# Kernel tuning notes

Measured on AMD Instinct MI355X. Metric: run time of the kernel, lower is better.

The kernel has to match this reference:

```python
import jax, jax.numpy as jnp
import numpy as np

B, S, D, H, AD, E = 4, 2048, 1024, 2048, 128, 8

def _ln(x, g, b, eps=1e-5):
    m = jnp.mean(x, axis=-1, keepdims=True)
    v = jnp.var(x, axis=-1, keepdims=True)
    return (x - m) * jax.lax.rsqrt(v + eps) * g + b

def setup_inputs() -> dict:
    key = jax.random.key(0)
    ks = jax.random.split(key, 12)
    scale = 1.0 / D ** 0.5
    ascale = scale * 0.01
    ead = 0.01 / AD ** 0.5
    return {
        'x': jax.random.normal(ks[0], (B, S, D), jnp.float32),
        'expert_weights': jax.random.uniform(ks[1], (B, S, E), jnp.float32),
        'Wu': jax.random.normal(ks[2], (H, D), jnp.float32) * scale,
        'bu': jnp.zeros((H,), jnp.float32),
        'Wg': jax.random.normal(ks[3], (H, D), jnp.float32) * scale,
        'bg': jnp.zeros((H,), jnp.float32),
        'Wd': jax.random.normal(ks[4], (D, H), jnp.float32) * scale,
        'bd': jnp.zeros((D,), jnp.float32),
        'Wpre': jax.random.normal(ks[5], (AD, D), jnp.float32) * ascale,
        'bpre': jnp.zeros((AD,), jnp.float32),
        'Wpost': jax.random.normal(ks[6], (AD, H), jnp.float32) * ascale,
        'bpost': jnp.zeros((AD,), jnp.float32),
        'ln_g': jnp.ones((AD,), jnp.float32),
        'ln_b': jnp.zeros((AD,), jnp.float32),
        'Wap': jax.random.normal(ks[7], (H, AD), jnp.float32) * ascale,
        'A': jax.random.normal(ks[8], (E, AD, AD), jnp.float32) * ead,
        'eg': jnp.ones((E, AD), jnp.float32),
        'eb': jnp.zeros((E, AD), jnp.float32),
        'Wp': jax.random.normal(ks[9], (H, AD), jnp.float32) * ead,
        'Wo': jax.random.normal(ks[10], (D, H), jnp.float32) * ead,
    }

def reference(x, expert_weights, Wu, bu, Wg, bg, Wd, bd, Wpre, bpre, Wpost, bpost, ln_g, ln_b, Wap, A, eg, eb, Wp, Wo):
    # ---- SharedExpertMLP ----
    up = x @ Wu.T + bu                      # [B,S,H]
    gate = x @ Wg.T + bg
    hidden = jax.nn.silu(gate) * up
    adapt_in = _ln(x @ Wpre.T + bpre, ln_g, ln_b)        # [B,S,AD]
    adapt_out = _ln(hidden @ Wpost.T + bpost, ln_g, ln_b)
    aw = jnp.einsum('bsa,bta->bst', adapt_in, adapt_out)  # [B,S,S]
    aw = jax.nn.silu(jnp.clip(aw, -5.0, 5.0))
    adapt = jnp.einsum('bst,bta->bsa', aw, adapt_in)
    hidden = hidden + 0.1 * (adapt @ Wap.T)
    shared = hidden @ Wd.T + bd                           # [B,S,D]
    # ---- expert branch (vectorized over experts) ----
    pre = x @ Wpre.T + bpre                               # [B,S,AD] (no adapt_norm here, as in torch)
    h = jnp.einsum('bsa,eca->ebsc', pre, A)               # per-expert adapter linear
    h = _ln(h, eg[:, None, None, :], eb[:, None, None, :])
    wmask = jnp.where(expert_weights > 0, expert_weights, 0.0)  # [B,S,E]
    hw = jnp.einsum('ebsa,bse->bsa', h, wmask)            # weighted combine before shared projections
    Wc = Wo @ Wp                                          # [D,AD]: output_proj(expert_proj(.))
    contrib = hw @ Wc.T                                   # [B,S,D]
    # sum_i w_i * (shared + 0.1*mask_i*expert_i) = shared*sum(w) + 0.1*sum(w_i*expert_i)
    return shared * jnp.sum(expert_weights, axis=-1, keepdims=True) + 0.1 * contrib
```

## Files before the change

### kernel.cpp

```cpp
#include <hip/hip_runtime.h>
#include <math.h>

#define BB 4
#define SS 2048
#define DD 1024
#define HH 2048
#define AD 128
#define EE 8
#define MM (BB*SS)
#define PS 136

typedef unsigned short u16;
typedef short bf16x8 __attribute__((ext_vector_type(8)));
typedef float f32x4 __attribute__((ext_vector_type(4)));
typedef float f32x16 __attribute__((ext_vector_type(16)));

__device__ __forceinline__ float silu_f(float x){ return x / (1.f + __expf(-x)); }

__device__ __forceinline__ u16 f2bf(float f){
    union { float f; unsigned u; } c; c.f = f;
    unsigned r = (c.u + 0x7FFFu + ((c.u >> 16) & 1u)) >> 16;
    return (u16)r;
}

__device__ __forceinline__ void gld16(const u16* g, u16* l){
    __builtin_amdgcn_global_load_lds((const __attribute__((address_space(1))) void*)g,
                                     (__attribute__((address_space(3))) void*)l, 16, 0, 0);
}

#define VMCNT(n) asm volatile("s_waitcnt vmcnt(" #n ")" ::: "memory")

__global__ __launch_bounds__(256,2) void mfma_sk(
    const u16* __restrict__ A, const u16* __restrict__ B, float* __restrict__ P,
    int M, int K, int S, long sA, long sB, long sC, long sSplit)
{
    __shared__ __align__(16) u16 As[128*32];
    __shared__ __align__(16) u16 Bs[128*32];
    const int t = threadIdx.x;
    const int lane = t & 63;
    const int wv = t >> 6;
    const int s = blockIdx.x;
    const int m0 = blockIdx.y * 128;
    const u16* Ab = A + (long)blockIdx.z * sA;
    const u16* Bb = B + (long)blockIdx.z * sB;
    const int srow = t >> 2, scol = (t & 3) * 8;
    const int Ks = K / S, kBeg = s * Ks;
    const u16* ga0 = Ab + (long)(m0 + srow) * K + scol + kBeg;
    const u16* ga1 = ga0 + 64L * K;
    const u16* gb0 = Bb + (long)srow * K + scol + kBeg;
    const u16* gb1 = gb0 + 64L * K;
    u16* la0 = As + t * 8;  u16* la1 = As + 2048 + t * 8;
    u16* lb0 = Bs + t * 8;  u16* lb1 = Bs + 2048 + t * 8;
    const int fr = lane & 15, q = lane >> 4;
    const int wm = (wv & 1) * 64, wn = (wv >> 1) * 64;

    f32x4 acc[4][4] = {};
    for (int k0 = 0; k0 < Ks; k0 += 32) {
        gld16(ga0 + k0, la0);
        gld16(ga1 + k0, la1);
        gld16(gb0 + k0, lb0);
        gld16(gb1 + k0, lb1);
        __syncthreads();
        bf16x8 af[4], bfr[4];
        #pragma unroll
        for (int i = 0; i < 4; ++i) af[i]  = *(const bf16x8*)&As[(wm + i*16 + fr)*32 + q*8];
        #pragma unroll
        for (int i = 0; i < 4; ++i) bfr[i] = *(const bf16x8*)&Bs[(wn + i*16 + fr)*32 + q*8];
        #pragma unroll
        for (int mi = 0; mi < 4; ++mi)
            #pragma unroll
            for (int ni = 0; ni < 4; ++ni)
                acc[mi][ni] = __builtin_amdgcn_mfma_f32_16x16x32_bf16(af[mi], bfr[ni], acc[mi][ni], 0, 0, 0);
        __syncthreads();
    }

    float* Pf = P + (long)s * sSplit + (long)blockIdx.z * sC;
    #pragma unroll
    for (int mi = 0; mi < 4; ++mi)
        #pragma unroll
        for (int ni = 0; ni < 4; ++ni) {
            const int col = wn + ni*16 + fr;
            #pragma unroll
            for (int r = 0; r < 4; ++r) {
                const int row = m0 + wm + mi*16 + q*4 + r;
                Pf[(long)row * 128 + col] = acc[mi][ni][r];
            }
        }
}

__global__ __launch_bounds__(512,2) void mfma_upgate(
    const u16* __restrict__ X, const u16* __restrict__ Wu_, const u16* __restrict__ Wg_,
    const float* __restrict__ bu, const float* __restrict__ bg, u16* __restrict__ H)
{
    __shared__ __align__(16) u16 lds[65536];
    const int t = threadIdx.x, lane = t & 63, wv = t >> 6;
    const int l31 = lane & 31, kh = lane >> 5;
    const int wr = wv >> 2, wc = wv & 3;
    const int m0 = blockIdx.y * 256, n0 = blockIdx.x * 128;

    const int srow = t >> 2;
    const int gcol = (((t & 3) ^ ((t >> 3) & 3)) * 8);
    const u16* gx0 = X   + (long)(m0 + srow) * DD + gcol;
    const u16* gx1 = gx0 + 128L * DD;
    const u16* gu  = Wu_ + (long)(n0 + srow) * DD + gcol;
    const u16* gg  = Wg_ + (long)(n0 + srow) * DD + gcol;
    const int st8 = t * 8;

    const int sw3 = (l31 >> 1) & 3;
    int offA[4][2], offB[2];
    #pragma unroll
    for (int m = 0; m < 4; ++m)
        #pragma unroll
        for (int ks = 0; ks < 2; ++ks)
            offA[m][ks] = (wr*128 + m*32 + l31)*32 + (((ks*2 + kh) ^ sw3) * 8);
    #pragma unroll
    for (int ks = 0; ks < 2; ++ks)
        offB[ks] = (wc*32 + l31)*32 + (((ks*2 + kh) ^ sw3) * 8);

    f32x16 accU[4] = {};
    f32x16 accG[4] = {};

    auto stage = [&](int tb) {
        u16* Lb = lds + (tb & 3) * 16384;
        const int k0 = tb * 32;
        gld16(gx0 + k0, Lb + st8);
        gld16(gx1 + k0, Lb + 4096 + st8);
        gld16(gu  + k0, Lb + 8192 + st8);
        gld16(gg  + k0, Lb + 12288 + st8);
    };

    auto compute = [&](int tb) {
        const u16* Lb = lds + (tb & 3) * 16384;
        bf16x8 a[4][2], uf[2], gf[2];
        #pragma unroll
        for (int ks = 0; ks < 2; ++ks) {
            uf[ks] = *(const bf16x8*)&Lb[8192  + offB[ks]];
            gf[ks] = *(const bf16x8*)&Lb[12288 + offB[ks]];
        }
        #pragma unroll
        for (int m = 0; m < 4; ++m)
            #pragma unroll
            for (int ks = 0; ks < 2; ++ks)
                a[m][ks] = *(const bf16x8*)&Lb[offA[m][ks]];
        __builtin_amdgcn_s_setprio(1);
        #pragma unroll
        for (int m = 0; m < 4; ++m)
            #pragma unroll
            for (int ks = 0; ks < 2; ++ks) {
                accU[m] = __builtin_amdgcn_mfma_f32_32x32x16_bf16(a[m][ks], uf[ks], accU[m], 0, 0, 0);
                accG[m] = __builtin_amdgcn_mfma_f32_32x32x16_bf16(a[m][ks], gf[ks], accG[m], 0, 0, 0);
            }
        __builtin_amdgcn_s_setprio(0);
    };

    stage(0); stage(1); stage(2);

    #pragma unroll 1
    for (int tt = 0; tt < 29; ++tt) {
        VMCNT(8);
        __builtin_amdgcn_s_barrier();
        __builtin_amdgcn_sched_barrier(0);
        stage(tt + 3);
        compute(tt);
    }
    VMCNT(8);
    __builtin_amdgcn_s_barrier();
    __builtin_amdgcn_sched_barrier(0);
    compute(29);
    VMCNT(4);
    __builtin_amdgcn_s_barrier();
    __builtin_amdgcn_sched_barrier(0);
    compute(30);
    VMCNT(0);
    __builtin_amdgcn_s_barrier();
    __builtin_amdgcn_sched_barrier(0);
    compute(31);

    const int col = n0 + wc*32 + l31;
    const float bub = bu[col], bgb = bg[col];
    u16* Hp = H + (long)(m0 + wr*128) * HH + col;
    #pragma unroll
    for (int m = 0; m < 4; ++m)
        #pragma unroll
        for (int r = 0; r < 16; ++r) {
            const int rowl = m*32 + (r & 3) + 8*(r >> 2) + 4*kh;
            const float u = accU[m][r] + bub;
            const float g = accG[m][r] + bgb;
            Hp[(long)rowl * HH] = f2bf(silu_f(g) * u);
        }
}

__global__ __launch_bounds__(512,2) void mfma_final(
    const u16* __restrict__ Hh, const u16* __restrict__ Wd_,
    const u16* __restrict__ Ac, const u16* __restrict__ Wcat,
    const float* __restrict__ bd, const float* __restrict__ sumw,
    float* __restrict__ out)
{
    __shared__ __align__(16) u16 lds[49152];
    const int t = threadIdx.x, lane = t & 63, wv = t >> 6;
    const int l31 = lane & 31, kh = lane >> 5;
    const int wr = wv >> 2, wc = wv & 3;
    const int m0 = blockIdx.y * 256, n0 = blockIdx.x * 128;

    const int r0 = t >> 2;
    const int gcol = (((t & 3) ^ ((t >> 3) & 3)) * 8);
    const u16* gA1 = Hh   + (long)(m0 + r0) * HH  + gcol;
    const u16* gB1 = Wd_  + (long)(n0 + r0) * HH  + gcol;
    const u16* gA2 = Ac   + (long)(m0 + r0) * 256 + gcol;
    const u16* gB2 = Wcat + (long)(n0 + r0) * 256 + gcol;
    const int st8 = t * 8;

    const int sw3 = (l31 >> 1) & 3;
    int offA[4][2], offB[2];
    #pragma unroll
    for (int m = 0; m < 4; ++m)
        #pragma unroll
        for (int ks = 0; ks < 2; ++ks)
            offA[m][ks] = (wr*128 + m*32 + l31)*32 + (((ks*2 + kh) ^ sw3) * 8);
    #pragma unroll
    for (int ks = 0; ks < 2; ++ks)
        offB[ks] = 8192 + (wc*32 + l31)*32 + (((ks*2 + kh) ^ sw3) * 8);

    f32x16 acc[4]  = {};
    f32x16 acc2[4] = {};

    auto stage = [&](int tk) {
        u16* Lb = lds + (tk & 3) * 12288;
        if (tk < 64) {
            const int k0 = tk * 32;
            gld16(gA1 + k0,             Lb + st8);
            gld16(gA1 + 128L*HH + k0,   Lb + 4096 + st8);
            gld16(gB1 + k0,             Lb + 8192 + st8);
        } else {
            const int k0 = (tk - 64) * 32;
            gld16(gA2 + k0,             Lb + st8);
            gld16(gA2 + 128L*256 + k0,  Lb + 4096 + st8);
            gld16(gB2 + k0,             Lb + 8192 + st8);
        }
    };

    auto compute = [&](int tk, f32x16 (&A)[4]) {
        const u16* Lb = lds + (tk & 3) * 12288;
        bf16x8 a[4][2], b[2];
        #pragma unroll
        for (int ks = 0; ks < 2; ++ks) b[ks] = *(const bf16x8*)&Lb[offB[ks]];
        #pragma unroll
        for (int m = 0; m < 4; ++m)
            #pragma unroll
            for (int ks = 0; ks < 2; ++ks)
                a[m][ks] = *(const bf16x8*)&Lb[offA[m][ks]];
        __builtin_amdgcn_s_setprio(1);
        #pragma unroll
        for (int m = 0; m < 4; ++m)
            #pragma unroll
            for (int ks = 0; ks < 2; ++ks)
                A[m] = __builtin_amdgcn_mfma_f32_32x32x16_bf16(a[m][ks], b[ks], A[m], 0, 0, 0);
        __builtin_amdgcn_s_setprio(0);
    };

    stage(0); stage(1); stage(2);
    #pragma unroll 1
    for (int tt = 0; tt < 69; ++tt) {
        VMCNT(6);
        __builtin_amdgcn_s_barrier();
        __builtin_amdgcn_sched_barrier(0);
        stage(tt + 3);
        if (tt < 64) compute(tt, acc); else compute(tt, acc2);
    }
    VMCNT(6);
    __builtin_amdgcn_s_barrier();
    __builtin_amdgcn_sched_barrier(0);
    compute(69, acc2);
    VMCNT(3);
    __builtin_amdgcn_s_barrier();
    __builtin_amdgcn_sched_barrier(0);
    compute(70, acc2);
    VMCNT(0);
    __builtin_amdgcn_s_barrier();
    __builtin_amdgcn_sched_barrier(0);
    compute(71, acc2);

    const int col = n0 + wc*32 + l31;
    const float bdc = bd[col];
    #pragma unroll
    for (int m = 0; m < 4; ++m)
        #pragma unroll
        for (int r = 0; r < 16; ++r) {
            const int row = m0 + wr*128 + m*32 + (r & 3) + 8*(r >> 2) + 4*kh;
            out[(long)row * DD + col] =
                sumw[row] * (acc[m][r] + bdc) + 0.1f * acc2[m][r];
        }
}

__global__ __launch_bounds__(256,2) void flash_pv(
    const u16* __restrict__ ai, const u16* __restrict__ ao,
    const u16* __restrict__ aiT, float* __restrict__ adaptP)
{
    __shared__ __align__(16) u16 As[128*32];
    __shared__ __align__(16) u16 Bs[128*32];
    __shared__ __align__(16) u16 Psh[128*PS];
    const int t = threadIdx.x, lane = t & 63, wv = t >> 6;
    const int fr = lane & 15, q = lane >> 4;
    const int wm = (wv & 1) * 64, wn = (wv >> 1) * 64;
    const int tg = blockIdx.x, s0 = blockIdx.y * 128, b = blockIdx.z;
    const u16* aib  = ai  + (long)b * SS * AD;
    const u16* aob  = ao  + (long)b * SS * AD;
    const u16* aiTb = aiT + (long)b * AD * SS;
    const int srow = t >> 2, scol = (t & 3) * 8;
    u16* la0 = As + t * 8;  u16* la1 = As + 2048 + t * 8;
    u16* lb0 = Bs + t * 8;  u16* lb1 = Bs + 2048 + t * 8;
    const u16* ga0 = aib + (long)(s0 + srow) * AD + scol;
    const u16* ga1 = ga0 + 64L * AD;

    f32x4 vacc[4][4] = {};
    for (int ti = 0; ti < 2; ++ti) {
        const int t0 = tg * 256 + ti * 128;
        const u16* gb0 = aob + (long)(t0 + srow) * AD + scol;
        const u16* gb1 = gb0 + 64L * AD;
        f32x4 acc[4][4] = {};
        for (int k0 = 0; k0 < AD; k0 += 32) {
            gld16(ga0 + k0, la0);
            gld16(ga1 + k0, la1);
            gld16(gb0 + k0, lb0);
            gld16(gb1 + k0, lb1);
            __syncthreads();
            bf16x8 af[4], bfr[4];
            #pragma unroll
            for (int i = 0; i < 4; ++i) af[i]  = *(const bf16x8*)&As[(wm + i*16 + fr)*32 + q*8];
            #pragma unroll
            for (int i = 0; i < 4; ++i) bfr[i] = *(const bf16x8*)&Bs[(wn + i*16 + fr)*32 + q*8];
            #pragma unroll
            for (int mi = 0; mi < 4; ++mi)
                #pragma unroll
                for (int ni = 0; ni < 4; ++ni)
                    acc[mi][ni] = __builtin_amdgcn_mfma_f32_16x16x32_bf16(af[mi], bfr[ni], acc[mi][ni], 0, 0, 0);
            __syncthreads();
        }
        #pragma unroll
        for (int mi = 0; mi < 4; ++mi)
            #pragma unroll
            for (int ni = 0; ni < 4; ++ni)
                #pragma unroll
                for (int r = 0; r < 4; ++r) {
                    float v = acc[mi][ni][r];
                    v = fminf(fmaxf(v, -5.f), 5.f);
                    Psh[(wm + mi*16 + q*4 + r)*PS + wn + ni*16 + fr] = f2bf(silu_f(v));
                }
        __syncthreads();
        #pragma unroll
        for (int kk = 0; kk < 4; ++kk) {
            bf16x8 pf[4], bi[4];
            #pragma unroll
            for (int mi = 0; mi < 4; ++mi)
                pf[mi] = *(const bf16x8*)&Psh[(wm + mi*16 + fr)*PS + kk*32 + q*8];
            #pragma unroll
            for (int ni = 0; ni < 4; ++ni)
                bi[ni] = *(const bf16x8*)&aiTb[(long)(wn + ni*16 + fr)*SS + t0 + kk*32 + q*8];
            #pragma unroll
            for (int mi = 0; mi < 4; ++mi)
                #pragma unroll
                for (int ni = 0; ni < 4; ++ni)
                    vacc[mi][ni] = __builtin_amdgcn_mfma_f32_16x16x32_bf16(pf[mi], bi[ni], vacc[mi][ni], 0, 0, 0);
        }
    }
    float* Pf = adaptP + (long)tg * MM * AD + (long)(b * SS + s0) * AD;
    #pragma unroll
    for (int mi = 0; mi < 4; ++mi)
        #pragma unroll
        for (int ni = 0; ni < 4; ++ni) {
            const int col = wn + ni*16 + fr;
            #pragma unroll
            for (int r = 0; r < 4; ++r) {
                const int row = wm + mi*16 + q*4 + r;
                Pf[(long)row * AD + col] = vacc[mi][ni][r];
            }
        }
}

__global__ __launch_bounds__(256) void scale_adapt(
    const float* __restrict__ P, const float* __restrict__ sumw, u16* __restrict__ acat)
{
    const int i = blockIdx.x * 256 + threadIdx.x;
    float4 v = ((const float4*)P)[i];
    #pragma unroll
    for (int tg = 1; tg < 8; ++tg) {
        const float4 w = ((const float4*)P)[i + (long)tg * (MM*AD/4)];
        v.x += w.x; v.y += w.y; v.z += w.z; v.w += w.w;
    }
    const long grow = i >> 5;
    const float sw = sumw[grow];
    ushort4 o;
    o.x = f2bf(sw*v.x); o.y = f2bf(sw*v.y); o.z = f2bf(sw*v.z); o.w = f2bf(sw*v.w);
    ((ushort4*)acat)[grow*64 + 32 + (i & 31)] = o;
}

__global__ __launch_bounds__(256) void expert_fused(
    const u16* __restrict__ pre, const u16* __restrict__ aexp,
    const float* __restrict__ ew, const float* __restrict__ eg,
    const float* __restrict__ eb, u16* __restrict__ acat,
    float* __restrict__ sumw)
{
    __shared__ float ewsh[64*8];
    __shared__ float egsh[8*128], ebsh[8*128];
    const int t = threadIdx.x, lane = t & 63, wv = t >> 6;
    const int fr = lane & 15, q = lane >> 4;
    const int wm = wv * 16;
    const int m0 = blockIdx.x * 64;
    if (t < 128) {
        const int row = t >> 1, j = (t & 1)*4;
        *(float4*)&ewsh[row*8+j] = *(const float4*)&ew[(long)(m0+row)*EE + j];
    }
    {   const int e = t >> 5, c = (t & 31)*4;
        *(float4*)&egsh[e*128+c] = *(const float4*)&eg[e*128+c];
        *(float4*)&ebsh[e*128+c] = *(const float4*)&eb[e*128+c]; }
    __syncthreads();

    f32x4 hwacc[8] = {};
    for (int e = 0; e < EE; ++e) {
        f32x4 acc[8] = {};
        const u16* Ae = aexp + (long)e * AD * AD;
        #pragma unroll
        for (int ks = 0; ks < 4; ++ks) {
            bf16x8 af, bfr[8];
            af = *(const bf16x8*)&pre[(long)(m0 + wm + fr)*AD + ks*32 + q*8];
            #pragma unroll
            for (int ni = 0; ni < 8; ++ni)
                bfr[ni] = *(const bf16x8*)&Ae[(long)(ni*16 + fr)*AD + ks*32 + q*8];
            #pragma unroll
            for (int ni = 0; ni < 8; ++ni)
                acc[ni] = __builtin_amdgcn_mfma_f32_16x16x32_bf16(af, bfr[ni], acc[ni], 0, 0, 0);
        }
        #pragma unroll
        for (int r = 0; r < 4; ++r) {
            float s = 0.f, s2 = 0.f;
            #pragma unroll
            for (int ni = 0; ni < 8; ++ni) { const float v = acc[ni][r]; s += v; s2 += v*v; }
            #pragma unroll
            for (int msk = 1; msk < 16; msk <<= 1) {
                s  += __shfl_xor(s,  msk, 64);
                s2 += __shfl_xor(s2, msk, 64);
            }
            const float mean = s * (1.f/128.f);
            const float var  = s2 * (1.f/128.f) - mean*mean;
            const float rs   = rsqrtf(var + 1e-5f);
            const int rowl = wm + q*4 + r;
            float w = ewsh[rowl*8 + e]; w = w > 0.f ? w : 0.f;
            #pragma unroll
            for (int ni = 0; ni < 8; ++ni) {
                const int col = ni*16 + fr;
                hwacc[ni][r] += w * ((acc[ni][r] - mean) * rs * egsh[e*128+col] + ebsh[e*128+col]);
            }
        }
    }
    #pragma unroll
    for (int r = 0; r < 4; ++r) {
        const int rowl = wm + q*4 + r;
        #pragma unroll
        for (int ni = 0; ni < 8; ++ni)
            acat[(long)(m0+rowl)*256 + ni*16 + fr] = f2bf(hwacc[ni][r]);
        if (fr == 0) {
            float sw = 0.f;
            #pragma unroll
            for (int j = 0; j < 8; ++j) sw += ewsh[rowl*8 + j];
            sumw[m0 + rowl] = sw;
        }
    }
}

template<int S>
__global__ __launch_bounds__(128) void ln_reduce(
    const float* __restrict__ P, long sSplit, const float* __restrict__ bias,
    u16* __restrict__ raw, u16* __restrict__ ln_out,
    const float* __restrict__ g, const float* __restrict__ b)
{
    const int r = blockIdx.x, tid = threadIdx.x;
    float v = bias[tid];
    #pragma unroll
    for (int s = 0; s < S; ++s) v += P[(long)s * sSplit + (long)r * AD + tid];
    if (raw) raw[(long)r * AD + tid] = f2bf(v);
    __shared__ float red[AD], red2[AD];
    red[tid] = v; red2[tid] = v*v;
    __syncthreads();
    for (int s = 64; s > 0; s >>= 1) {
        if (tid < s) { red[tid] += red[tid+s]; red2[tid] += red2[tid+s]; }
        __syncthreads();
    }
    const float mean = red[0] * (1.f/AD);
    const float var  = red2[0] * (1.f/AD) - mean*mean;
    const float rs   = rsqrtf(var + 1e-5f);
    ln_out[(long)r * AD + tid] = f2bf((v - mean) * rs * g[tid] + b[tid]);
}

__global__ __launch_bounds__(256) void reduce_cat(
    const float* __restrict__ P, u16* __restrict__ Wcat)
{
    const int i = blockIdx.x * 256 + threadIdx.x;
    const int a4 = i & 31, z = (i >> 5) & 1, d = i >> 6;
    const float* src = P + (long)z * (4L*DD*AD) + (long)d * AD + a4*4;
    float4 v = *(const float4*)src;
    #pragma unroll
    for (int s = 1; s < 4; ++s) {
        const float4 w = *(const float4*)(src + (long)s * DD * AD);
        v.x += w.x; v.y += w.y; v.z += w.z; v.w += w.w;
    }
    ushort4 o; o.x=f2bf(v.x); o.y=f2bf(v.y); o.z=f2bf(v.z); o.w=f2bf(v.w);
    ((ushort4*)Wcat)[(long)d*64 + z*32 + a4] = o;
}

__global__ __launch_bounds__(256) void transpose6(
    const u16* __restrict__ wRaw, u16* __restrict__ wT,
    const u16* __restrict__ ai, u16* __restrict__ aiT)
{
    __shared__ u16 tile[32][33];
    const int z = blockIdx.z;
    const u16* in; u16* out;
    if (z < 2) { in = wRaw + (long)z * HH * AD; out = wT + (long)z * AD * HH; }
    else       { in = ai + (long)(z-2) * SS * AD; out = aiT + (long)(z-2) * AD * SS; }
    const int x0 = blockIdx.x * 32, y0 = blockIdx.y * 32;
    const int tx = threadIdx.x & 31, ty = threadIdx.x >> 5;
    #pragma unroll
    for (int j = 0; j < 4; ++j)
        tile[ty + j*8][tx] = in[(long)(y0 + ty + j*8) * AD + x0 + tx];
    __syncthreads();
    #pragma unroll
    for (int j = 0; j < 4; ++j)
        out[(long)(x0 + ty + j*8) * SS + y0 + tx] = tile[tx][ty + j*8];
}

struct Cvt5 { const float* in[5]; u16* out[5]; long cum[6]; };
__global__ __launch_bounds__(256) void cvt_pack(Cvt5 a)
{
    const long i = (long)blockIdx.x * 256 + threadIdx.x;
    if (i >= a.cum[5]) return;
    int s = 0;
    while (i >= a.cum[s+1]) ++s;
    const long j = i - a.cum[s];
    const float4 v = ((const float4*)a.in[s])[j];
    ushort4 o;
    o.x = f2bf(v.x); o.y = f2bf(v.y); o.z = f2bf(v.z); o.w = f2bf(v.w);
    ((ushort4*)a.out[s])[j] = o;
}

extern "C" void kernel_launch(void* const* d_in, const int* in_sizes, int n_in,
                              void* d_out, int out_size, void* d_ws, size_t ws_size,
                              hipStream_t stream) {
    const float* x    = (const float*)d_in[0];
    const float* ew   = (const float*)d_in[1];
    const float* Wu   = (const float*)d_in[2];
    const float* bu   = (const float*)d_in[3];
    const float* Wg   = (const float*)d_in[4];
    const float* bg   = (const float*)d_in[5];
    const float* Wd   = (const float*)d_in[6];
    const float* bd   = (const float*)d_in[7];
    const float* Wpre = (const float*)d_in[8];
    const float* bpre = (const float*)d_in[9];
    const float* Wpost= (const float*)d_in[10];
    const float* bpost= (const float*)d_in[11];
    const float* ln_g = (const float*)d_in[12];
    const float* ln_b = (const float*)d_in[13];
    const float* Wap  = (const float*)d_in[14];
    const float* Aex  = (const float*)d_in[15];
    const float* eg   = (const float*)d_in[16];
    const float* eb   = (const float*)d_in[17];
    const float* Wp   = (const float*)d_in[18];
    const float* Wo   = (const float*)d_in[19];
    float* out = (float*)d_out;

    char* p = (char*)d_ws;
    auto take = [&](long bytes) -> char* {
        char* r = p; p += (bytes + 255) & ~255L; return r;
    };
    u16* x_slot  = (u16*)take(16777216);
    u16* wslot   = (u16*)take((long)2*DD*HH*2);
    u16* wpre    = (u16*)take((long)AD*DD*2);
    u16* aex     = (u16*)take((long)EE*AD*AD*2);
    u16* pre_bf  = (u16*)take((long)MM*AD*2);
    u16* ai_bf   = (u16*)take((long)MM*AD*2);
    char* shareA = take(33554432);
    u16* acat    = (u16*)take((long)MM*256*2);
    float* sumw  = (float*)take((long)MM*4);
    u16* hidden  = (u16*)take((long)MM*HH*2);

    u16* x_bf    = x_slot;
    u16* aiT     = x_slot;
    u16* wRaw    = aiT  + 1048576;
    u16* wT      = wRaw + 524288;
    u16* wpost_w = wT   + 524288;
    u16* wcat    = wpost_w + 262144;
    u16* ao_bf   = wcat + 262144;
    float* wcP   = (float*)(ao_bf + 1048576);
    float* preP   = (float*)shareA;
    float* wpostP = (float*)shareA;
    float* adaptP = (float*)shareA;

    {
        Cvt5 a;
        a.in[0]=x;    a.out[0]=x_bf;              long n0=(long)MM*DD/4;
        a.in[1]=Wu;   a.out[1]=wslot;             long n1=(long)HH*DD/4;
        a.in[2]=Wg;   a.out[2]=wslot+(long)DD*HH; long n2=(long)HH*DD/4;
        a.in[3]=Wpre; a.out[3]=wpre;              long n3=(long)AD*DD/4;
        a.in[4]=Aex;  a.out[4]=aex;               long n4=(long)EE*AD*AD/4;
        a.cum[0]=0; a.cum[1]=n0; a.cum[2]=n0+n1; a.cum[3]=n0+n1+n2;
        a.cum[4]=n0+n1+n2+n3; a.cum[5]=n0+n1+n2+n3+n4;
        cvt_pack<<<dim3((a.cum[5]+255)/256), 256, 0, stream>>>(a);
    }
    mfma_sk<<<dim3(4, MM/128, 1), 256, 0, stream>>>(
        x_bf, wpre, preP, MM, DD, 4, 0, 0, 0, (long)MM*AD);
    ln_reduce<4><<<dim3(MM), 128, 0, stream>>>(preP, (long)MM*AD, bpre, pre_bf, ai_bf, ln_g, ln_b);
    expert_fused<<<dim3(MM/64), 256, 0, stream>>>(pre_bf, aex, ew, eg, eb, acat, sumw);
    mfma_upgate<<<dim3(HH/128, MM/256), 512, 0, stream>>>(
        x_bf, wslot, wslot+(long)DD*HH, bu, bg, hidden);
    {
        Cvt5 a;
        a.in[0]=Wo;    a.out[0]=wslot;             long n0=(long)DD*HH/4;
        a.in[1]=Wd;    a.out[1]=wslot+(long)DD*HH; long n1=(long)DD*HH/4;
        a.in[2]=Wpost; a.out[2]=wpost_w;           long n2=(long)AD*HH/4;
        a.in[3]=Wp;    a.out[3]=wRaw;              long n3=(long)HH*AD/4;
        a.in[4]=Wap;   a.out[4]=wRaw+(long)HH*AD;  long n4=(long)HH*AD/4;
        a.cum[0]=0; a.cum[1]=n0; a.cum[2]=n0+n1; a.cum[3]=n0+n1+n2;
        a.cum[4]=n0+n1+n2+n3; a.cum[5]=n0+n1+n2+n3+n4;
        cvt_pack<<<dim3((a.cum[5]+255)/256), 256, 0, stream>>>(a);
    }
    transpose6<<<dim3(4,64,6), 256, 0, stream>>>(wRaw, wT, ai_bf, aiT);
    mfma_sk<<<dim3(4, DD/128, 2), 256, 0, stream>>>(
        wslot, wT, wcP, DD, HH, 4, (long)DD*HH, (long)AD*HH, 4L*DD*AD, (long)DD*AD);
    reduce_cat<<<dim3(256), 256, 0, stream>>>(wcP, wcat);
    mfma_sk<<<dim3(8, MM/128, 1), 256, 0, stream>>>(
        hidden, wpost_w, wpostP, MM, HH, 8, 0, 0, 0, (long)MM*AD);
    ln_reduce<8><<<dim3(MM), 128, 0, stream>>>(wpostP, (long)MM*AD, bpost, nullptr, ao_bf, ln_g, ln_b);
    flash_pv<<<dim3(8, SS/128, BB), 256, 0, stream>>>(ai_bf, ao_bf, aiT, adaptP);
    scale_adapt<<<dim3((long)MM*AD/4/256), 256, 0, stream>>>(adaptP, sumw, acat);
    mfma_final<<<dim3(DD/128, MM/256), 512, 0, stream>>>(
        hidden, wslot+(long)DD*HH, acat, wcat, bd, sumw, out);
}
```

Baseline: 424.2 us.

## Shrink GEMM tiles, split expert loop across waves, raise split-K for Wc

The up/gate and final GEMMs move from 256x128 tiles with 512 threads and a 4-stage LDS pipeline to 128x128 tiles with 256 threads and a 3-stage pipeline. Each wave now computes a 2x2 grid of 32x32 MFMA outputs, so the grid has more blocks and each block uses less LDS. The expert kernel halves rows per block and splits the 8 experts across two wave groups, combining their partial sums through shared memory. The Wc = Wo@Wp split-K GEMM goes from 4 to 16 splits, with reduce_cat summing 16 partials. The trade is more parallelism and occupancy against less operand reuse per tile, more global traffic and extra partial-sum work.

Result: faster. 398.4 us (-6.1%).

```diff
diff --git a/kernel.cpp b/kernel.cpp
--- a/kernel.cpp
+++ b/kernel.cpp
@@ -88,86 +88,87 @@
         }
 }
 
-__global__ __launch_bounds__(512,2) void mfma_upgate(
+__global__ __launch_bounds__(256,2) void mfma_upgate(
     const u16* __restrict__ X, const u16* __restrict__ Wu_, const u16* __restrict__ Wg_,
     const float* __restrict__ bu, const float* __restrict__ bg, u16* __restrict__ H)
 {
-    __shared__ __align__(16) u16 lds[65536];
+    __shared__ __align__(16) u16 lds[36864];
     const int t = threadIdx.x, lane = t & 63, wv = t >> 6;
     const int l31 = lane & 31, kh = lane >> 5;
-    const int wr = wv >> 2, wc = wv & 3;
-    const int m0 = blockIdx.y * 256, n0 = blockIdx.x * 128;
+    const int wr = wv & 1, wc = wv >> 1;
+    const int m0 = blockIdx.y * 128, n0 = blockIdx.x * 128;
 
     const int srow = t >> 2;
     const int gcol = (((t & 3) ^ ((t >> 3) & 3)) * 8);
-    const u16* gx0 = X   + (long)(m0 + srow) * DD + gcol;
-    const u16* gx1 = gx0 + 128L * DD;
-    const u16* gu  = Wu_ + (long)(n0 + srow) * DD + gcol;
-    const u16* gg  = Wg_ + (long)(n0 + srow) * DD + gcol;
+    const u16* gx = X   + (long)(m0 + srow) * DD + gcol;
+    const u16* gu = Wu_ + (long)(n0 + srow) * DD + gcol;
+    const u16* gg = Wg_ + (long)(n0 + srow) * DD + gcol;
     const int st8 = t * 8;
 
     const int sw3 = (l31 >> 1) & 3;
-    int offA[4][2], offB[2];
-    #pragma unroll
-    for (int m = 0; m < 4; ++m)
-        #pragma unroll
-        for (int ks = 0; ks < 2; ++ks)
-            offA[m][ks] = (wr*128 + m*32 + l31)*32 + (((ks*2 + kh) ^ sw3) * 8);
-    #pragma unroll
-    for (int ks = 0; ks < 2; ++ks)
-        offB[ks] = (wc*32 + l31)*32 + (((ks*2 + kh) ^ sw3) * 8);
-
-    f32x16 accU[4] = {};
-    f32x16 accG[4] = {};
+    int offA[2][2], offU[2][2], offG[2][2];
+    #pragma unroll
+    for (int m = 0; m < 2; ++m)
+        #pragma unroll
+        for (int ks = 0; ks < 2; ++ks) {
+            const int ko = ((ks*2 + kh) ^ sw3) * 8;
+            offA[m][ks] =        (wr*64 + m*32 + l31)*32 + ko;
+            offU[m][ks] = 4096 + (wc*64 + m*32 + l31)*32 + ko;
+            offG[m][ks] = 8192 + (wc*64 + m*32 + l31)*32 + ko;
+        }
+
+    f32x16 accU[2][2] = {};
+    f32x16 accG[2][2] = {};
 
     auto stage = [&](int tb) {
-        u16* Lb = lds + (tb & 3) * 16384;
+        u16* Lb = lds + (tb % 3) * 12288;
         const int k0 = tb * 32;
-        gld16(gx0 + k0, Lb + st8);
-        gld16(gx1 + k0, Lb + 4096 + st8);
-        gld16(gu  + k0, Lb + 8192 + st8);
-        gld16(gg  + k0, Lb + 12288 + st8);
+        gld16(gx + k0,           Lb + st8);
+        gld16(gx + 64L*DD + k0,  Lb + 2048 + st8);
+        gld16(gu + k0,           Lb + 4096 + st8);
+        gld16(gu + 64L*DD + k0,  Lb + 6144 + st8);
+        gld16(gg + k0,           Lb + 8192 + st8);
+        gld16(gg + 64L*DD + k0,  Lb + 10240 + st8);
     };
 
     auto compute = [&](int tb) {
-        const u16* Lb = lds + (tb & 3) * 16384;
-        bf16x8 a[4][2], uf[2], gf[2];
-        #pragma unroll
-        for (int ks = 0; ks < 2; ++ks) {
-            uf[ks] = *(const bf16x8*)&Lb[8192  + offB[ks]];
-            gf[ks] = *(const bf16x8*)&Lb[12288 + offB[ks]];
-        }
-        #pragma unroll
-        for (int m = 0; m < 4; ++m)
+        const u16* Lb = lds + (tb % 3) * 12288;
+        bf16x8 a[2][2], uf[2][2], gf[2][2];
+        #pragma unroll
+        for (int n = 0; n < 2; ++n)
+            #pragma unroll
+            for (int ks = 0; ks < 2; ++ks) {
+                uf[n][ks] = *(const bf16x8*)&Lb[offU[n][ks]];
+                gf[n][ks] = *(const bf16x8*)&Lb[offG[n][ks]];
+            }
+        #pragma unroll
+        for (int m = 0; m < 2; ++m)
             #pragma unroll
             for (int ks = 0; ks < 2; ++ks)
                 a[m][ks] = *(const bf16x8*)&Lb[offA[m][ks]];
         __builtin_amdgcn_s_setprio(1);
         #pragma unroll
-        for (int m = 0; m < 4; ++m)
-            #pragma unroll
-            for (int ks = 0; ks < 2; ++ks) {
-                accU[m] = __builtin_amdgcn_mfma_f32_32x32x16_bf16(a[m][ks], uf[ks], accU[m], 0, 0, 0);
-                accG[m] = __builtin_amdgcn_mfma_f32_32x32x16_bf16(a[m][ks], gf[ks], accG[m], 0, 0, 0);
-            }
+        for (int m = 0; m < 2; ++m)
+            #pragma unroll
+            for (int n = 0; n < 2; ++n)
+                #pragma unroll
+                for (int ks = 0; ks < 2; ++ks) {
+                    accU[m][n] = __builtin_amdgcn_mfma_f32_32x32x16_bf16(a[m][ks], uf[n][ks], accU[m][n], 0, 0, 0);
+                    accG[m][n] = __builtin_amdgcn_mfma_f32_32x32x16_bf16(a[m][ks], gf[n][ks], accG[m][n], 0, 0, 0);
+                }
         __builtin_amdgcn_s_setprio(0);
     };
 
-    stage(0); stage(1); stage(2);
-
+    stage(0); stage(1);
     #pragma unroll 1
-    for (int tt = 0; tt < 29; ++tt) {
-        VMCNT(8);
+    for (int tt = 0; tt < 30; ++tt) {
+        VMCNT(6);
         __builtin_amdgcn_s_barrier();
         __builtin_amdgcn_sched_barrier(0);
-        stage(tt + 3);
+        stage(tt + 2);
         compute(tt);
     }
-    VMCNT(8);
-    __builtin_amdgcn_s_barrier();
-    __builtin_amdgcn_sched_barrier(0);
-    compute(29);
-    VMCNT(4);
+    VMCNT(6);
     __builtin_amdgcn_s_barrier();
     __builtin_amdgcn_sched_barrier(0);
     compute(30);
@@ -176,102 +177,104 @@
     __builtin_amdgcn_sched_barrier(0);
     compute(31);
 
-    const int col = n0 + wc*32 + l31;
-    const float bub = bu[col], bgb = bg[col];
-    u16* Hp = H + (long)(m0 + wr*128) * HH + col;
-    #pragma unroll
-    for (int m = 0; m < 4; ++m)
-        #pragma unroll
-        for (int r = 0; r < 16; ++r) {
-            const int rowl = m*32 + (r & 3) + 8*(r >> 2) + 4*kh;
-            const float u = accU[m][r] + bub;
-            const float g = accG[m][r] + bgb;
-            Hp[(long)rowl * HH] = f2bf(silu_f(g) * u);
-        }
-}
-
-__global__ __launch_bounds__(512,2) void mfma_final(
+    #pragma unroll
+    for (int n = 0; n < 2; ++n) {
+        const int col = n0 + wc*64 + n*32 + l31;
+        const float bub = bu[col], bgb = bg[col];
+        #pragma unroll
+        for (int m = 0; m < 2; ++m)
+            #pragma unroll
+            for (int r = 0; r < 16; ++r) {
+                const int row = m0 + wr*64 + m*32 + (r & 3) + 8*(r >> 2) + 4*kh;
+                const float u = accU[m][n][r] + bub;
+                const float g = accG[m][n][r] + bgb;
+                H[(long)row * HH + col] = f2bf(silu_f(g) * u);
+            }
+    }
+}
+
+__global__ __launch_bounds__(256,2) void mfma_final(
     const u16* __restrict__ Hh, const u16* __restrict__ Wd_,
     const u16* __restrict__ Ac, const u16* __restrict__ Wcat,
     const float* __restrict__ bd, const float* __restrict__ sumw,
     float* __restrict__ out)
 {
-    __shared__ __align__(16) u16 lds[49152];
+    __shared__ __align__(16) u16 lds[24576];
     const int t = threadIdx.x, lane = t & 63, wv = t >> 6;
     const int l31 = lane & 31, kh = lane >> 5;
-    const int wr = wv >> 2, wc = wv & 3;
-    const int m0 = blockIdx.y * 256, n0 = blockIdx.x * 128;
-
-    const int r0 = t >> 2;
+    const int wr = wv & 1, wc = wv >> 1;
+    const int m0 = blockIdx.y * 128, n0 = blockIdx.x * 128;
+
+    const int srow = t >> 2;
     const int gcol = (((t & 3) ^ ((t >> 3) & 3)) * 8);
-    const u16* gA1 = Hh   + (long)(m0 + r0) * HH  + gcol;
-    const u16* gB1 = Wd_  + (long)(n0 + r0) * HH  + gcol;
-    const u16* gA2 = Ac   + (long)(m0 + r0) * 256 + gcol;
-    const u16* gB2 = Wcat + (long)(n0 + r0) * 256 + gcol;
+    const u16* gA1 = Hh   + (long)(m0 + srow) * HH  + gcol;
+    const u16* gB1 = Wd_  + (long)(n0 + srow) * HH  + gcol;
+    const u16* gA2 = Ac   + (long)(m0 + srow) * 256 + gcol;
+    const u16* gB2 = Wcat + (long)(n0 + srow) * 256 + gcol;
     const int st8 = t * 8;
 
     const int sw3 = (l31 >> 1) & 3;
-    int offA[4][2], offB[2];
-    #pragma unroll
-    for (int m = 0; m < 4; ++m)
-        #pragma unroll
-        for (int ks = 0; ks < 2; ++ks)
-            offA[m][ks] = (wr*128 + m*32 + l31)*32 + (((ks*2 + kh) ^ sw3) * 8);
-    #pragma unroll
-    for (int ks = 0; ks < 2; ++ks)
-        offB[ks] = 8192 + (wc*32 + l31)*32 + (((ks*2 + kh) ^ sw3) * 8);
-
-    f32x16 acc[4]  = {};
-    f32x16 acc2[4] = {};
+    int offA[2][2], offB[2][2];
+    #pragma unroll
+    for (int m = 0; m < 2; ++m)
+        #pragma unroll
+        for (int ks = 0; ks < 2; ++ks) {
+            const int ko = ((ks*2 + kh) ^ sw3) * 8;
+            offA[m][ks] =        (wr*64 + m*32 + l31)*32 + ko;
+            offB[m][ks] = 4096 + (wc*64 + m*32 + l31)*32 + ko;
+        }
+
+    f32x16 acc[2][2]  = {};
+    f32x16 acc2[2][2] = {};
 
     auto stage = [&](int tk) {
-        u16* Lb = lds + (tk & 3) * 12288;
+        u16* Lb = lds + (tk % 3) * 8192;
         if (tk < 64) {
             const int k0 = tk * 32;
-            gld16(gA1 + k0,             Lb + st8);
-            gld16(gA1 + 128L*HH + k0,   Lb + 4096 + st8);
-            gld16(gB1 + k0,             Lb + 8192 + st8);
+            gld16(gA1 + k0,           Lb + st8);
+            gld16(gA1 + 64L*HH + k0,  Lb + 2048 + st8);
+            gld16(gB1 + k0,           Lb + 4096 + st8);
+            gld16(gB1 + 64L*HH + k0,  Lb + 6144 + st8);
         } else {
             const int k0 = (tk - 64) * 32;
-            gld16(gA2 + k0,             Lb + st8);
-            gld16(gA2 + 128L*256 + k0,  Lb + 4096 + st8);
-            gld16(gB2 + k0,             Lb + 8192 + st8);
+            gld16(gA2 + k0,           Lb + st8);
+            gld16(gA2 + 64L*256 + k0, Lb + 2048 + st8);
+            gld16(gB2 + k0,           Lb + 4096 + st8);
+            gld16(gB2 + 64L*256 + k0, Lb + 6144 + st8);
         }
     };
 
-    auto compute = [&](int tk, f32x16 (&A)[4]) {
-        const u16* Lb = lds + (tk & 3) * 12288;
-        bf16x8 a[4][2], b[2];
-        #pragma unroll
-        for (int ks = 0; ks < 2; ++ks) b[ks] = *(const bf16x8*)&Lb[offB[ks]];
-        #pragma unroll
-        for (int m = 0; m < 4; ++m)
-            #pragma unroll
-            for (int ks = 0; ks < 2; ++ks)
+    auto compute = [&](int tk, f32x16 (&A)[2][2]) {
+        const u16* Lb = lds + (tk % 3) * 8192;
+        bf16x8 a[2][2], b[2][2];
+        #pragma unroll
+        for (int m = 0; m < 2; ++m)
+            #pragma unroll
+            for (int ks = 0; ks < 2; ++ks) {
                 a[m][ks] = *(const bf16x8*)&Lb[offA[m][ks]];
+                b[m][ks] = *(const bf16x8*)&Lb[offB[m][ks]];
+            }
         __builtin_amdgcn_s_setprio(1);
         #pragma unroll
-        for (int m = 0; m < 4; ++m)
-            #pragma unroll
-            for (int ks = 0; ks < 2; ++ks)
-                A[m] = __builtin_amdgcn_mfma_f32_32x32x16_bf16(a[m][ks], b[ks], A[m], 0, 0, 0);
+        for (int m = 0; m < 2; ++m)
+            #pragma unroll
+            for (int n = 0; n < 2; ++n)
+                #pragma unroll
+                for (int ks = 0; ks < 2; ++ks)
+                    A[m][n] = __builtin_amdgcn_mfma_f32_32x32x16_bf16(a[m][ks], b[n][ks], A[m][n], 0, 0, 0);
         __builtin_amdgcn_s_setprio(0);
     };
 
-    stage(0); stage(1); stage(2);
+    stage(0); stage(1);
     #pragma unroll 1
-    for (int tt = 0; tt < 69; ++tt) {
-        VMCNT(6);
+    for (int tt = 0; tt < 70; ++tt) {
+        VMCNT(4);
         __builtin_amdgcn_s_barrier();
         __builtin_amdgcn_sched_barrier(0);
-        stage(tt + 3);
+        stage(tt + 2);
         if (tt < 64) compute(tt, acc); else compute(tt, acc2);
     }
-    VMCNT(6);
-    __builtin_amdgcn_s_barrier();
-    __builtin_amdgcn_sched_barrier(0);
-    compute(69, acc2);
-    VMCNT(3);
+    VMCNT(4);
     __builtin_amdgcn_s_barrier();
     __builtin_amdgcn_sched_barrier(0);
     compute(70, acc2);
@@ -280,16 +283,19 @@
     __builtin_amdgcn_sched_barrier(0);
     compute(71, acc2);
 
-    const int col = n0 + wc*32 + l31;
-    const float bdc = bd[col];
-    #pragma unroll
-    for (int m = 0; m < 4; ++m)
-        #pragma unroll
-        for (int r = 0; r < 16; ++r) {
-            const int row = m0 + wr*128 + m*32 + (r & 3) + 8*(r >> 2) + 4*kh;
-            out[(long)row * DD + col] =
-                sumw[row] * (acc[m][r] + bdc) + 0.1f * acc2[m][r];
-        }
+    #pragma unroll
+    for (int n = 0; n < 2; ++n) {
+        const int col = n0 + wc*64 + n*32 + l31;
+        const float bdc = bd[col];
+        #pragma unroll
+        for (int m = 0; m < 2; ++m)
+            #pragma unroll
+            for (int r = 0; r < 16; ++r) {
+                const int row = m0 + wr*64 + m*32 + (r & 3) + 8*(r >> 2) + 4*kh;
+                out[(long)row * DD + col] =
+                    sumw[row] * (acc[m][n][r] + bdc) + 0.1f * acc2[m][n][r];
+            }
+    }
 }
 
 __global__ __launch_bounds__(256,2) void flash_pv(
@@ -400,13 +406,15 @@
     const float* __restrict__ eb, u16* __restrict__ acat,
     float* __restrict__ sumw)
 {
-    __shared__ float ewsh[64*8];
+    __shared__ float ewsh[32*8];
     __shared__ float egsh[8*128], ebsh[8*128];
+    __shared__ float part[32*132];
     const int t = threadIdx.x, lane = t & 63, wv = t >> 6;
     const int fr = lane & 15, q = lane >> 4;
-    const int wm = wv * 16;
-    const int m0 = blockIdx.x * 64;
-    if (t < 128) {
+    const int wm = (wv & 1) * 16;
+    const int e0 = (wv >> 1) * 4;
+    const int m0 = blockIdx.x * 32;
+    if (t < 64) {
         const int row = t >> 1, j = (t & 1)*4;
         *(float4*)&ewsh[row*8+j] = *(const float4*)&ew[(long)(m0+row)*EE + j];
     }
@@ -416,7 +424,8 @@
     __syncthreads();
 
     f32x4 hwacc[8] = {};
-    for (int e = 0; e < EE; ++e) {
+    for (int ee = 0; ee < 4; ++ee) {
+        const int e = e0 + ee;
         f32x4 acc[8] = {};
         const u16* Ae = aexp + (long)e * AD * AD;
         #pragma unroll
@@ -452,17 +461,31 @@
             }
         }
     }
-    #pragma unroll
-    for (int r = 0; r < 4; ++r) {
-        const int rowl = wm + q*4 + r;
-        #pragma unroll
-        for (int ni = 0; ni < 8; ++ni)
-            acat[(long)(m0+rowl)*256 + ni*16 + fr] = f2bf(hwacc[ni][r]);
-        if (fr == 0) {
-            float sw = 0.f;
-            #pragma unroll
-            for (int j = 0; j < 8; ++j) sw += ewsh[rowl*8 + j];
-            sumw[m0 + rowl] = sw;
+    if (wv >= 2) {
+        #pragma unroll
+        for (int r = 0; r < 4; ++r) {
+            const int rowl = wm + q*4 + r;
+            #pragma unroll
+            for (int ni = 0; ni < 8; ++ni)
+                part[rowl*132 + ni*16 + fr] = hwacc[ni][r];
+        }
+    }
+    __syncthreads();
+    if (wv < 2) {
+        #pragma unroll
+        for (int r = 0; r < 4; ++r) {
+            const int rowl = wm + q*4 + r;
+            #pragma unroll
+            for (int ni = 0; ni < 8; ++ni) {
+                const float v = hwacc[ni][r] + part[rowl*132 + ni*16 + fr];
+                acat[(long)(m0+rowl)*256 + ni*16 + fr] = f2bf(v);
+            }
+            if (fr == 0) {
+                float sw = 0.f;
+                #pragma unroll
+                for (int j = 0; j < 8; ++j) sw += ewsh[rowl*8 + j];
+                sumw[m0 + rowl] = sw;
+            }
         }
     }
 }
@@ -496,10 +519,10 @@
 {
     const int i = blockIdx.x * 256 + threadIdx.x;
     const int a4 = i & 31, z = (i >> 5) & 1, d = i >> 6;
-    const float* src = P + (long)z * (4L*DD*AD) + (long)d * AD + a4*4;
+    const float* src = P + (long)z * (16L*DD*AD) + (long)d * AD + a4*4;
     float4 v = *(const float4*)src;
     #pragma unroll
-    for (int s = 1; s < 4; ++s) {
+    for (int s = 1; s < 16; ++s) {
         const float4 w = *(const float4*)(src + (long)s * DD * AD);
         v.x += w.x; v.y += w.y; v.z += w.z; v.w += w.w;
     }
@@ -588,8 +611,8 @@
     u16* wpost_w = wT   + 524288;
     u16* wcat    = wpost_w + 262144;
     u16* ao_bf   = wcat + 262144;
-    float* wcP   = (float*)(ao_bf + 1048576);
     float* preP   = (float*)shareA;
+    float* wcP    = (float*)(shareA + 16777216);
     float* wpostP = (float*)shareA;
     float* adaptP = (float*)shareA;
 
@@ -607,8 +630,8 @@
     mfma_sk<<<dim3(4, MM/128, 1), 256, 0, stream>>>(
         x_bf, wpre, preP, MM, DD, 4, 0, 0, 0, (long)MM*AD);
     ln_reduce<4><<<dim3(MM), 128, 0, stream>>>(preP, (long)MM*AD, bpre, pre_bf, ai_bf, ln_g, ln_b);
-    expert_fused<<<dim3(MM/64), 256, 0, stream>>>(pre_bf, aex, ew, eg, eb, acat, sumw);
-    mfma_upgate<<<dim3(HH/128, MM/256), 512, 0, stream>>>(
+    expert_fused<<<dim3(MM/32), 256, 0, stream>>>(pre_bf, aex, ew, eg, eb, acat, sumw);
+    mfma_upgate<<<dim3(HH/128, MM/128), 256, 0, stream>>>(
         x_bf, wslot, wslot+(long)DD*HH, bu, bg, hidden);
     {
         Cvt5 a;
@@ -622,14 +645,14 @@
         cvt_pack<<<dim3((a.cum[5]+255)/256), 256, 0, stream>>>(a);
     }
     transpose6<<<dim3(4,64,6), 256, 0, stream>>>(wRaw, wT, ai_bf, aiT);
-    mfma_sk<<<dim3(4, DD/128, 2), 256, 0, stream>>>(
-        wslot, wT, wcP, DD, HH, 4, (long)DD*HH, (long)AD*HH, 4L*DD*AD, (long)DD*AD);
+    mfma_sk<<<dim3(16, DD/128, 2), 256, 0, stream>>>(
+        wslot, wT, wcP, DD, HH, 16, (long)DD*HH, (long)AD*HH, 16L*DD*AD, (long)DD*AD);
     reduce_cat<<<dim3(256), 256, 0, stream>>>(wcP, wcat);
     mfma_sk<<<dim3(8, MM/128, 1), 256, 0, stream>>>(
         hidden, wpost_w, wpostP, MM, HH, 8, 0, 0, 0, (long)MM*AD);
     ln_reduce<8><<<dim3(MM), 128, 0, stream>>>(wpostP, (long)MM*AD, bpost, nullptr, ao_bf, ln_g, ln_b);
     flash_pv<<<dim3(8, SS/128, BB), 256, 0, stream>>>(ai_bf, ao_bf, aiT, adaptP);
     scale_adapt<<<dim3((long)MM*AD/4/256), 256, 0, stream>>>(adaptP, sumw, acat);
-    mfma_final<<<dim3(DD/128, MM/256), 512, 0, stream>>>(
+    mfma_final<<<dim3(DD/128, MM/128), 256, 0, stream>>>(
         hidden, wslot+(long)DD*HH, acat, wcat, bd, sumw, out);
 }
```
